# Performance work log

Hardware: AMD Instinct MI355X
Metric: run time of the kernel (lower is better)

Reference implementation:

```python
import jax, jax.numpy as jnp
import numpy as np

HEADS = 8

def setup_inputs() -> dict:
    key = jax.random.key(0)
    ks = jax.random.split(key, 7)
    B, N, M, C = 4, 2048, 2048, 512
    s = 0.02
    return {
        "hidden_states": jax.random.normal(ks[0], (B, N, C), jnp.float32),
        "encoder_states": jax.random.normal(ks[1], (B, M, C), jnp.float32),
        "Wq": jax.random.normal(ks[2], (C, C), jnp.float32) * s,
        "Wk": jax.random.normal(ks[3], (C, C), jnp.float32) * s,
        "Wv": jax.random.normal(ks[4], (C, C), jnp.float32) * s,
        "Wo": jax.random.normal(ks[5], (C, C), jnp.float32) * s,
        "bo": jnp.zeros((C,), jnp.float32),
    }

def reference(hidden_states, encoder_states, Wq, Wk, Wv, Wo, bo):
    B, N, C = hidden_states.shape
    M = encoder_states.shape[1]
    H = HEADS
    dh = C // H
    scale = dh ** -0.5  # q.shape[-1] ** -0.5 in FlashAttentionFunction / attn.scale
    # projections (to_q/to_k/to_v, no bias as in diffusers CrossAttention)
    q = (hidden_states @ Wq).reshape(B, N, H, dh).transpose(0, 2, 1, 3)   # [B,H,N,dh]
    k = (encoder_states @ Wk).reshape(B, M, H, dh).transpose(0, 2, 1, 3)  # [B,H,M,dh]
    v = (encoder_states @ Wv).reshape(B, M, H, dh).transpose(0, 2, 1, 3)  # [B,H,M,dh]
    # baddbmm(scores) -> softmax -> bmm(values); no mask, non-causal
    scores = jnp.einsum('bhnd,bhmd->bhnm', q, k) * scale                  # [B,H,N,M]
    probs = jax.nn.softmax(scores, axis=-1)
    out = jnp.einsum('bhnm,bhmd->bhnd', probs, v)                         # [B,H,N,dh]
    out = out.transpose(0, 2, 1, 3).reshape(B, N, C)                      # batch_to_head_dim
    return out @ Wo + bo                                                  # to_out[0]; to_out[1] is dropout (identity at eval)
```

## Files before the change

kernel.cpp:

```cpp
#include <hip/hip_runtime.h>
#include <stdint.h>
#include <stddef.h>

typedef __bf16 bf16x8 __attribute__((ext_vector_type(8)));
typedef float f32x4 __attribute__((ext_vector_type(4)));
typedef float f32x16 __attribute__((ext_vector_type(16)));
typedef int int4v __attribute__((ext_vector_type(4)));
typedef unsigned short u16;
typedef unsigned int u32;

__device__ __forceinline__ u16 f2bf(float f) {
    union { float f; unsigned u; } x; x.f = f;
    unsigned r = x.u + 0x7fffu + ((x.u >> 16) & 1u);
    return (u16)(r >> 16);
}

__device__ __forceinline__ float fexp2(float x) { return __builtin_amdgcn_exp2f(x); }

__device__ __forceinline__ u32 cvtpk(float lo, float hi) {
    u32 r;
    asm("v_cvt_pk_bf16_f32 %0, %1, %2" : "=v"(r) : "v"(lo), "v"(hi));
    return r;
}

__device__ __forceinline__ void perm32swap(u32& a, u32& b) {
    asm("v_permlane32_swap_b32 %0, %1" : "+v"(a), "+v"(b));
}

__device__ __forceinline__ f32x16 mfma32(bf16x8 a, bf16x8 b, f32x16 c) {
    return __builtin_amdgcn_mfma_f32_32x32x16_bf16(a, b, c, 0, 0, 0);
}

__device__ __forceinline__ void gl16(const void* g, void* l) {
    __builtin_amdgcn_global_load_lds(
        (const __attribute__((address_space(1))) void*)g,
        (__attribute__((address_space(3))) void*)l, 16, 0, 0);
}

__global__ __launch_bounds__(256) void wtrans4(
        const float* __restrict__ Wq, const float* __restrict__ Wk,
        const float* __restrict__ Wv, const float* __restrict__ Wo,
        u16* __restrict__ oq, u16* __restrict__ ok,
        u16* __restrict__ ov, u16* __restrict__ oo) {
    const int z = blockIdx.z;
    const float* W = (z == 0) ? Wq : (z == 1) ? Wk : (z == 2) ? Wv : Wo;
    u16* O = (z == 0) ? oq : (z == 1) ? ok : (z == 2) ? ov : oo;
    int t  = blockIdx.x * 256 + threadIdx.x;
    int g  = t >> 12;
    int k0 = (t >> 9) & 7;
    int n  = t & 511;
    float v[8];
#pragma unroll
    for (int j = 0; j < 8; ++j)
        v[j] = W[(size_t)(k0 * 64 + g * 8 + j) * 512 + n];
    int gs = g ^ (n & 7);
    u16* dst = O + ((size_t)(k0 * 512 + n) * 8 + gs) * 8;
    ushort4 a, b;
    a.x = f2bf(v[0]); a.y = f2bf(v[1]); a.z = f2bf(v[2]); a.w = f2bf(v[3]);
    b.x = f2bf(v[4]); b.y = f2bf(v[5]); b.z = f2bf(v[6]); b.w = f2bf(v[7]);
    *(ushort4*)dst = a;
    *(ushort4*)(dst + 4) = b;
}

__global__ __launch_bounds__(256) void gemm_qkv(
        const float* __restrict__ hidden, const float* __restrict__ enc,
        const u16* __restrict__ wq, const u16* __restrict__ wk, const u16* __restrict__ wv,
        u16* __restrict__ qo, u16* __restrict__ ko, u16* __restrict__ vo) {
    __shared__ __align__(16) u16 As[128 * 64];
    __shared__ __align__(16) u16 Bs[128 * 64];
    const int z = blockIdx.z;
    const float* A = (z == 0) ? hidden : enc;
    const u16* Bp = (z == 0) ? wq : (z == 1) ? wk : wv;
    const int tid = threadIdx.x, lane = tid & 63, wave = tid >> 6;
    const int wr = (wave >> 1) * 64, wc = (wave & 1) * 64;
    const int brow = blockIdx.x * 128, bcol = blockIdx.y * 128;
    const int lrow = lane & 15;
    const int sr = tid >> 3, sc = tid & 7;

    f32x4 acc[4][4] = {};

    for (int k0s = 0; k0s < 8; ++k0s) {
        const u16* bsrc = Bp + ((size_t)(k0s * 512 + bcol) * 64) + (size_t)(wave * 256 + lane) * 8;
#pragma unroll
        for (int i = 0; i < 4; ++i)
            gl16(bsrc + i * 512, (char*)Bs + wave * 4096 + i * 1024);
#pragma unroll
        for (int i = 0; i < 4; ++i) {
            int r = i * 32 + sr;
            const float* src = A + (size_t)(brow + r) * 512 + k0s * 64 + sc * 8;
            float4 f0 = *(const float4*)src, f1 = *(const float4*)(src + 4);
            int4v w;
            w[0] = cvtpk(f0.x, f0.y); w[1] = cvtpk(f0.z, f0.w);
            w[2] = cvtpk(f1.x, f1.y); w[3] = cvtpk(f1.z, f1.w);
            *(int4v*)((char*)As + r * 128 + ((sc ^ (r & 7)) << 4)) = w;
        }
        __syncthreads();
#pragma unroll
        for (int kc = 0; kc < 2; ++kc) {
            const int kg = kc * 4 + (lane >> 4);
            bf16x8 af[4], bfr[4];
#pragma unroll
            for (int m = 0; m < 4; ++m) {
                int r = wr + m * 16 + lrow;
                af[m] = *(const bf16x8*)((char*)As + r * 128 + ((kg ^ (r & 7)) << 4));
            }
#pragma unroll
            for (int n = 0; n < 4; ++n) {
                int r = wc + n * 16 + lrow;
                bfr[n] = *(const bf16x8*)((char*)Bs + r * 128 + ((kg ^ (r & 7)) << 4));
            }
#pragma unroll
            for (int m = 0; m < 4; ++m)
#pragma unroll
                for (int n = 0; n < 4; ++n)
                    acc[m][n] = __builtin_amdgcn_mfma_f32_16x16x32_bf16(af[m], bfr[n], acc[m][n], 0, 0, 0);
        }
        __syncthreads();
    }

#pragma unroll
    for (int m = 0; m < 4; ++m) {
        int gr0 = brow + wr + m * 16 + ((lane >> 4) << 2);
#pragma unroll
        for (int n = 0; n < 4; ++n) {
            int gc = bcol + wc + n * 16 + lrow;
            int hh = gc >> 6, d = gc & 63;
            if (z == 2) {
                int b = gr0 >> 11, mm = gr0 & 2047;
                ushort4 pk;
                pk.x = f2bf(acc[m][n][0]); pk.y = f2bf(acc[m][n][1]);
                pk.z = f2bf(acc[m][n][2]); pk.w = f2bf(acc[m][n][3]);
                *(ushort4*)(vo + ((size_t)(b * 8 + hh) * 64 + d) * 2048 + mm) = pk;
            } else {
                u16* dst = (z == 0) ? qo : ko;
                const float s = (z == 0) ? 0.125f * 1.44269504f : 1.0f;
#pragma unroll
                for (int j = 0; j < 4; ++j) {
                    int gr = gr0 + j;
                    int b = gr >> 11, nn = gr & 2047;
                    dst[((size_t)(b * 8 + hh) * 2048 + nn) * 64 + d] = f2bf(acc[m][n][j] * s);
                }
            }
        }
    }
}

__global__ __launch_bounds__(256) void gemm_out(
        const u16* __restrict__ A, const u16* __restrict__ Bp,
        const float* __restrict__ bias, float* __restrict__ out) {
    __shared__ __align__(16) u16 As[128 * 64];
    __shared__ __align__(16) u16 Bs[64 * 64];
    const int tid = threadIdx.x, lane = tid & 63, wave = tid >> 6;
    const int wr = (wave >> 1) * 64, wc = (wave & 1) * 32;
    const int brow = blockIdx.x * 128, bcol = blockIdx.y * 64;
    const int lrow = lane & 15;
    const int ar = wave * 32 + (lane >> 3), ag = lane & 7;

    f32x4 acc[4][2] = {};

    for (int k0s = 0; k0s < 8; ++k0s) {
        const u16* asrc = A + (size_t)(brow + ar) * 512 + k0s * 64 + ag * 8;
#pragma unroll
        for (int i = 0; i < 4; ++i)
            gl16(asrc + (size_t)(i * 8) * 512, (char*)As + wave * 4096 + i * 1024);
        const u16* bsrc = Bp + ((size_t)(k0s * 512 + bcol) * 64) + (size_t)(wave * 128 + lane) * 8;
#pragma unroll
        for (int i = 0; i < 2; ++i)
            gl16(bsrc + i * 512, (char*)Bs + wave * 2048 + i * 1024);
        __syncthreads();
#pragma unroll
        for (int kc = 0; kc < 2; ++kc) {
            const int kg = kc * 4 + (lane >> 4);
            bf16x8 af[4], bfr[2];
#pragma unroll
            for (int m = 0; m < 4; ++m) {
                int r = wr + m * 16 + lrow;
                af[m] = *(const bf16x8*)((char*)As + r * 128 + ((kg ^ (r & 7)) << 4));
            }
#pragma unroll
            for (int n = 0; n < 2; ++n) {
                int r = wc + n * 16 + lrow;
                bfr[n] = *(const bf16x8*)((char*)Bs + r * 128 + ((kg ^ (r & 7)) << 4));
            }
#pragma unroll
            for (int m = 0; m < 4; ++m)
#pragma unroll
                for (int n = 0; n < 2; ++n)
                    acc[m][n] = __builtin_amdgcn_mfma_f32_16x16x32_bf16(af[m], bfr[n], acc[m][n], 0, 0, 0);
        }
        __syncthreads();
    }

#pragma unroll
    for (int m = 0; m < 4; ++m) {
        int gr0 = brow + wr + m * 16 + ((lane >> 4) << 2);
#pragma unroll
        for (int n = 0; n < 2; ++n) {
            int gc = bcol + wc + n * 16 + lrow;
            float bv = bias[gc];
#pragma unroll
            for (int j = 0; j < 4; ++j)
                out[(size_t)(gr0 + j) * 512 + gc] = acc[m][n][j] + bv;
        }
    }
}

__global__ __launch_bounds__(256, 2) void flash_attn(
        const u16* __restrict__ Q, const u16* __restrict__ K,
        const u16* __restrict__ VT, u16* __restrict__ Oa) {
    __shared__ __align__(16) char smem[65536];

    const int tid  = threadIdx.x;
    const int lane = tid & 63;
    const int wave = tid >> 6;
    const int qg   = wave >> 1;
    const int half = wave & 1;
    const int ql   = lane & 31;
    const int hl   = lane >> 5;
    const int bid  = blockIdx.x;
    const int lid  = (bid & 7) * 64 + (bid >> 3);
    const int bh   = lid >> 4;
    const int qt   = lid & 15;
    const int qbase = qt * 128 + qg * 64;

    bf16x8 qf[2][4];
#pragma unroll
    for (int sq = 0; sq < 2; ++sq)
#pragma unroll
        for (int kc = 0; kc < 4; ++kc)
            qf[sq][kc] = *(const bf16x8*)(Q + ((size_t)bh * 2048 + qbase + sq * 32 + ql) * 64 + kc * 16 + hl * 8);

    const u16* Kb = K  + (size_t)bh * 131072 + ((size_t)half * 1024 + ql) * 64 + hl * 8;
    const u16* Vb = VT + (size_t)bh * 131072 + (size_t)ql * 2048 + half * 1024 + hl * 8;

#define STAGE(b_, t_) do { \
    if (qg == 0) { \
        const u16* s_ = Kb + (size_t)(t_) * 4096; \
        char* d_ = smem + (b_) * 32768 + half * 8192; \
        gl16(s_,             d_); \
        gl16(s_ + 16,        d_ + 1024); \
        gl16(s_ + 32,        d_ + 2048); \
        gl16(s_ + 48,        d_ + 3072); \
        gl16(s_ + 2048,      d_ + 4096); \
        gl16(s_ + 2048 + 16, d_ + 5120); \
        gl16(s_ + 2048 + 32, d_ + 6144); \
        gl16(s_ + 2048 + 48, d_ + 7168); \
    } else { \
        const u16* s_ = Vb + (t_) * 64; \
        char* d_ = smem + (b_) * 32768 + 16384 + half * 8192; \
        gl16(s_,              d_);           \
        gl16(s_ + 65536,      d_ + 1024);    \
        gl16(s_ + 16,         d_ + 2048);    \
        gl16(s_ + 16 + 65536, d_ + 3072);    \
        gl16(s_ + 32,         d_ + 4096);    \
        gl16(s_ + 32 + 65536, d_ + 5120);    \
        gl16(s_ + 48,         d_ + 6144);    \
        gl16(s_ + 48 + 65536, d_ + 7168);    \
    } \
} while (0)

    f32x16 acc00 = {}, acc01 = {}, acc10 = {}, acc11 = {};
    float ls[2][4] = {};

    STAGE(0, 0);
    __syncthreads();

    for (int t = 0; t < 16; ++t) {
        const int b = t & 1;
        if (t < 15) STAGE(b ^ 1, t + 1);

#pragma unroll
        for (int ks = 0; ks < 2; ++ks) {
            const u16* Kt = (const u16*)(smem + b * 32768 + half * 8192 + ks * 4096);
            const u16* Vt = (const u16*)(smem + b * 32768 + 16384 + half * 8192 + ks * 4096);
            bf16x8 kf[4], vf[2][2];
#pragma unroll
            for (int kc = 0; kc < 4; ++kc)
                kf[kc] = *(const bf16x8*)(Kt + kc * 512 + lane * 8);
#pragma unroll
            for (int jl = 0; jl < 2; ++jl)
#pragma unroll
                for (int dh2 = 0; dh2 < 2; ++dh2)
                    vf[jl][dh2] = *(const bf16x8*)(Vt + (jl * 2 + dh2) * 512 + lane * 8);

            f32x16 st0 = {}, st1 = {};
            __builtin_amdgcn_s_setprio(1);
#pragma unroll
            for (int kc = 0; kc < 4; ++kc) {
                st0 = mfma32(kf[kc], qf[0][kc], st0);
                st1 = mfma32(kf[kc], qf[1][kc], st1);
            }
            __builtin_amdgcn_s_setprio(0);

#pragma unroll
            for (int r = 0; r < 16; r += 4) {
                st0[r]   = fexp2(st0[r]);   ls[0][0] += st0[r];
                st0[r+1] = fexp2(st0[r+1]); ls[0][1] += st0[r+1];
                st0[r+2] = fexp2(st0[r+2]); ls[0][2] += st0[r+2];
                st0[r+3] = fexp2(st0[r+3]); ls[0][3] += st0[r+3];
                st1[r]   = fexp2(st1[r]);   ls[1][0] += st1[r];
                st1[r+1] = fexp2(st1[r+1]); ls[1][1] += st1[r+1];
                st1[r+2] = fexp2(st1[r+2]); ls[1][2] += st1[r+2];
                st1[r+3] = fexp2(st1[r+3]); ls[1][3] += st1[r+3];
            }

            __builtin_amdgcn_s_setprio(1);
#pragma unroll
            for (int jl = 0; jl < 2; ++jl) {
                u32 A0 = cvtpk(st0[8*jl+0], st0[8*jl+1]);
                u32 A1 = cvtpk(st0[8*jl+2], st0[8*jl+3]);
                u32 B0 = cvtpk(st0[8*jl+4], st0[8*jl+5]);
                u32 B1 = cvtpk(st0[8*jl+6], st0[8*jl+7]);
                perm32swap(A0, B0);
                perm32swap(A1, B1);
                union { bf16x8 v; u32 u[4]; } bb0;
                bb0.u[0] = A0; bb0.u[1] = A1; bb0.u[2] = B0; bb0.u[3] = B1;
                acc00 = mfma32(vf[jl][0], bb0.v, acc00);
                acc01 = mfma32(vf[jl][1], bb0.v, acc01);
                u32 C0 = cvtpk(st1[8*jl+0], st1[8*jl+1]);
                u32 C1 = cvtpk(st1[8*jl+2], st1[8*jl+3]);
                u32 D0 = cvtpk(st1[8*jl+4], st1[8*jl+5]);
                u32 D1 = cvtpk(st1[8*jl+6], st1[8*jl+7]);
                perm32swap(C0, D0);
                perm32swap(C1, D1);
                union { bf16x8 v; u32 u[4]; } bb1;
                bb1.u[0] = C0; bb1.u[1] = C1; bb1.u[2] = D0; bb1.u[3] = D1;
                acc10 = mfma32(vf[jl][0], bb1.v, acc10);
                acc11 = mfma32(vf[jl][1], bb1.v, acc11);
            }
            __builtin_amdgcn_s_setprio(0);
        }
        __syncthreads();
    }
#undef STAGE

    float lsum0 = (ls[0][0] + ls[0][1]) + (ls[0][2] + ls[0][3]);
    float lsum1 = (ls[1][0] + ls[1][1]) + (ls[1][2] + ls[1][3]);
    lsum0 += __shfl_xor(lsum0, 32);
    lsum1 += __shfl_xor(lsum1, 32);

    float* CB = (float*)smem;
    float* LS = (float*)(smem + 32768);

#define PUBQ(sq, A0, A1, LSV) do { \
    int qq = (sq) * 32 + ql; \
    float* R = CB + qg * 4096 + qq * 64; \
    _Pragma("unroll") \
    for (int rg = 0; rg < 4; ++rg) { \
        int g0 = (2 * rg + hl) ^ (qq & 15); \
        *(f32x4*)(R + g0 * 4) = f32x4{A0[4*rg], A0[4*rg+1], A0[4*rg+2], A0[4*rg+3]}; \
        int g1 = (8 + 2 * rg + hl) ^ (qq & 15); \
        *(f32x4*)(R + g1 * 4) = f32x4{A1[4*rg], A1[4*rg+1], A1[4*rg+2], A1[4*rg+3]}; \
    } \
    if (hl == 0) LS[qg * 64 + qq] = LSV; \
} while (0)

#define REDQ(sq, A0, A1, LSV) do { \
    int qq = (sq) * 32 + ql; \
    const float* R = CB + qg * 4096 + qq * 64; \
    _Pragma("unroll") \
    for (int rg = 0; rg < 4; ++rg) { \
        int g0 = (2 * rg + hl) ^ (qq & 15); \
        f32x4 v0 = *(const f32x4*)(R + g0 * 4); \
        A0[4*rg] += v0[0]; A0[4*rg+1] += v0[1]; A0[4*rg+2] += v0[2]; A0[4*rg+3] += v0[3]; \
        int g1 = (8 + 2 * rg + hl) ^ (qq & 15); \
        f32x4 v1 = *(const f32x4*)(R + g1 * 4); \
        A1[4*rg] += v1[0]; A1[4*rg+1] += v1[1]; A1[4*rg+2] += v1[2]; A1[4*rg+3] += v1[3]; \
    } \
    LSV += LS[qg * 64 + qq]; \
} while (0)

    if (half == 1) {
        PUBQ(0, acc00, acc01, lsum0);
        PUBQ(1, acc10, acc11, lsum1);
    }
    __syncthreads();
    if (half == 0) {
        REDQ(0, acc00, acc01, lsum0);
        REDQ(1, acc10, acc11, lsum1);
        float inv0 = 1.0f / lsum0, inv1 = 1.0f / lsum1;
        int b_ = bh >> 3, hd = bh & 7;
#define STOQ(sq, A0, A1, INV) do { \
        int qrow = qbase + (sq) * 32 + ql; \
        u16* orow = Oa + ((size_t)b_ * 2048 + qrow) * 512 + hd * 64; \
        _Pragma("unroll") \
        for (int rg = 0; rg < 4; ++rg) { \
            int d00 = ((rg ^ (qrow & 7)) << 3) + hl * 4; \
            ushort4 p0; \
            p0.x = f2bf(A0[4*rg] * INV);   p0.y = f2bf(A0[4*rg+1] * INV); \
            p0.z = f2bf(A0[4*rg+2] * INV); p0.w = f2bf(A0[4*rg+3] * INV); \
            *(ushort4*)(orow + d00) = p0; \
            int d01 = (((4 + rg) ^ (qrow & 7)) << 3) + hl * 4; \
            ushort4 p1; \
            p1.x = f2bf(A1[4*rg] * INV);   p1.y = f2bf(A1[4*rg+1] * INV); \
            p1.z = f2bf(A1[4*rg+2] * INV); p1.w = f2bf(A1[4*rg+3] * INV); \
            *(ushort4*)(orow + d01) = p1; \
        } \
} while (0)
        STOQ(0, acc00, acc01, inv0);
        STOQ(1, acc10, acc11, inv1);
#undef STOQ
    }
#undef PUBQ
#undef REDQ
}

extern "C" void kernel_launch(void* const* d_in, const int* in_sizes, int n_in,
                              void* d_out, int out_size, void* d_ws, size_t ws_size,
                              hipStream_t stream) {
    const float* hidden = (const float*)d_in[0];
    const float* enc    = (const float*)d_in[1];
    const float* Wq     = (const float*)d_in[2];
    const float* Wk     = (const float*)d_in[3];
    const float* Wv     = (const float*)d_in[4];
    const float* Wo     = (const float*)d_in[5];
    const float* bo     = (const float*)d_in[6];
    float* out = (float*)d_out;

    char* ws = (char*)d_ws;
    const size_t MB = 1ull << 20;
    u16* q_bf  = (u16*)(ws + 0 * MB);
    u16* k_bf  = (u16*)(ws + 8 * MB);
    u16* vt_bf = (u16*)(ws + 16 * MB);
    u16* at_bf = (u16*)(ws + 24 * MB);
    u16* wq_t  = (u16*)(ws + 32 * MB);
    u16* wk_t  = (u16*)(ws + 32 * MB + 512 * 1024);
    u16* wv_t  = (u16*)(ws + 33 * MB);
    u16* wo_t  = (u16*)(ws + 33 * MB + 512 * 1024);

    dim3 wg(128, 1, 4);
    wtrans4<<<wg, 256, 0, stream>>>(Wq, Wk, Wv, Wo, wq_t, wk_t, wv_t, wo_t);

    dim3 qkvg(64, 4, 3);
    gemm_qkv<<<qkvg, 256, 0, stream>>>(hidden, enc, wq_t, wk_t, wv_t, q_bf, k_bf, vt_bf);

    flash_attn<<<512, 256, 0, stream>>>(q_bf, k_bf, vt_bf, at_bf);

    dim3 og(64, 8);
    gemm_out<<<og, 256, 0, stream>>>(at_bf, wo_t, bo, out);
}
```

Measured before the change: 91.08 us.

## Pre-pack K and V into MFMA fragment layout and shrink attention LDS footprint

The QKV projection now writes K and V directly in the per-lane fragment order the attention kernel consumes, so each staging step is four contiguous 1KB copies per wave instead of strided gathers. The attention kernel halves its per-iteration tile (32 iterations of one sub-step), cutting shared memory from 64KB to about 33KB and raising launch bounds to allow four blocks per CU. This aims to improve global load coalescing and occupancy, at the cost of twice as many barriers and scattered 2-byte stores in the K write-out.

After: 220.3 us. +141.9%, slower.

```diff
diff --git a/kernel.cpp b/kernel.cpp
--- a/kernel.cpp
+++ b/kernel.cpp
@@ -125,21 +125,33 @@
         for (int n = 0; n < 4; ++n) {
             int gc = bcol + wc + n * 16 + lrow;
             int hh = gc >> 6, d = gc & 63;
-            if (z == 2) {
-                int b = gr0 >> 11, mm = gr0 & 2047;
+            int b = gr0 >> 11;
+            int bh2 = b * 8 + hh;
+            if (z == 0) {
+                int nn = gr0 & 2047;
+#pragma unroll
+                for (int j = 0; j < 4; ++j)
+                    qo[((size_t)bh2 * 2048 + nn + j) * 64 + d] =
+                        f2bf(acc[m][n][j] * (0.125f * 1.44269504f));
+            } else if (z == 1) {
+                int kc2 = d >> 4, hl2 = (d >> 3) & 1, e = d & 7;
+#pragma unroll
+                for (int j = 0; j < 4; ++j) {
+                    int nn = (gr0 & 2047) + j;
+                    size_t off = (((size_t)bh2 * 64 + (nn >> 5)) * 4 + kc2) * 512
+                               + (size_t)((nn & 31) + 32 * hl2) * 8 + e;
+                    ko[off] = f2bf(acc[m][n][j]);
+                }
+            } else {
+                int nn0 = gr0 & 2047;
+                int slice = ((nn0 >> 4) & 1) * 2 + (d >> 5);
+                int lanev = (d & 31) + 32 * ((nn0 >> 3) & 1);
+                size_t off = (((size_t)bh2 * 64 + (nn0 >> 5)) * 4 + slice) * 512
+                           + (size_t)lanev * 8 + (nn0 & 7);
                 ushort4 pk;
                 pk.x = f2bf(acc[m][n][0]); pk.y = f2bf(acc[m][n][1]);
                 pk.z = f2bf(acc[m][n][2]); pk.w = f2bf(acc[m][n][3]);
-                *(ushort4*)(vo + ((size_t)(b * 8 + hh) * 64 + d) * 2048 + mm) = pk;
-            } else {
-                u16* dst = (z == 0) ? qo : ko;
-                const float s = (z == 0) ? 0.125f * 1.44269504f : 1.0f;
-#pragma unroll
-                for (int j = 0; j < 4; ++j) {
-                    int gr = gr0 + j;
-                    int b = gr >> 11, nn = gr & 2047;
-                    dst[((size_t)(b * 8 + hh) * 2048 + nn) * 64 + d] = f2bf(acc[m][n][j] * s);
-                }
+                *(ushort4*)(vo + off) = pk;
             }
         }
     }
@@ -205,10 +217,10 @@
     }
 }
 
-__global__ __launch_bounds__(256, 2) void flash_attn(
-        const u16* __restrict__ Q, const u16* __restrict__ K,
-        const u16* __restrict__ VT, u16* __restrict__ Oa) {
-    __shared__ __align__(16) char smem[65536];
+__global__ __launch_bounds__(256, 4) void flash_attn(
+        const u16* __restrict__ KQ, const u16* __restrict__ KP,
+        const u16* __restrict__ VP, u16* __restrict__ Oa) {
+    __shared__ __align__(16) char smem[33280];
 
     const int tid  = threadIdx.x;
     const int lane = tid & 63;
@@ -228,35 +240,18 @@
     for (int sq = 0; sq < 2; ++sq)
 #pragma unroll
         for (int kc = 0; kc < 4; ++kc)
-            qf[sq][kc] = *(const bf16x8*)(Q + ((size_t)bh * 2048 + qbase + sq * 32 + ql) * 64 + kc * 16 + hl * 8);
-
-    const u16* Kb = K  + (size_t)bh * 131072 + ((size_t)half * 1024 + ql) * 64 + hl * 8;
-    const u16* Vb = VT + (size_t)bh * 131072 + (size_t)ql * 2048 + half * 1024 + hl * 8;
+            qf[sq][kc] = *(const bf16x8*)(KQ + ((size_t)bh * 2048 + qbase + sq * 32 + ql) * 64 + kc * 16 + hl * 8);
+
+    const u16* Pb = (qg == 0 ? KP : VP) + ((size_t)bh * 64 + half * 32) * 2048 + lane * 8;
+    char* dst0 = smem + half * 8192 + (qg == 0 ? 0 : 4096);
 
 #define STAGE(b_, t_) do { \
-    if (qg == 0) { \
-        const u16* s_ = Kb + (size_t)(t_) * 4096; \
-        char* d_ = smem + (b_) * 32768 + half * 8192; \
-        gl16(s_,             d_); \
-        gl16(s_ + 16,        d_ + 1024); \
-        gl16(s_ + 32,        d_ + 2048); \
-        gl16(s_ + 48,        d_ + 3072); \
-        gl16(s_ + 2048,      d_ + 4096); \
-        gl16(s_ + 2048 + 16, d_ + 5120); \
-        gl16(s_ + 2048 + 32, d_ + 6144); \
-        gl16(s_ + 2048 + 48, d_ + 7168); \
-    } else { \
-        const u16* s_ = Vb + (t_) * 64; \
-        char* d_ = smem + (b_) * 32768 + 16384 + half * 8192; \
-        gl16(s_,              d_);           \
-        gl16(s_ + 65536,      d_ + 1024);    \
-        gl16(s_ + 16,         d_ + 2048);    \
-        gl16(s_ + 16 + 65536, d_ + 3072);    \
-        gl16(s_ + 32,         d_ + 4096);    \
-        gl16(s_ + 32 + 65536, d_ + 5120);    \
-        gl16(s_ + 48,         d_ + 6144);    \
-        gl16(s_ + 48 + 65536, d_ + 7168);    \
-    } \
+    const u16* s_ = Pb + (size_t)(t_) * 2048; \
+    char* d_ = dst0 + (b_) * 16384; \
+    gl16(s_,        d_); \
+    gl16(s_ + 512,  d_ + 1024); \
+    gl16(s_ + 1024, d_ + 2048); \
+    gl16(s_ + 1536, d_ + 3072); \
 } while (0)
 
     f32x16 acc00 = {}, acc01 = {}, acc10 = {}, acc11 = {};
@@ -265,71 +260,69 @@
     STAGE(0, 0);
     __syncthreads();
 
-    for (int t = 0; t < 16; ++t) {
+    for (int t = 0; t < 32; ++t) {
         const int b = t & 1;
-        if (t < 15) STAGE(b ^ 1, t + 1);
-
-#pragma unroll
-        for (int ks = 0; ks < 2; ++ks) {
-            const u16* Kt = (const u16*)(smem + b * 32768 + half * 8192 + ks * 4096);
-            const u16* Vt = (const u16*)(smem + b * 32768 + 16384 + half * 8192 + ks * 4096);
-            bf16x8 kf[4], vf[2][2];
-#pragma unroll
-            for (int kc = 0; kc < 4; ++kc)
-                kf[kc] = *(const bf16x8*)(Kt + kc * 512 + lane * 8);
-#pragma unroll
-            for (int jl = 0; jl < 2; ++jl)
-#pragma unroll
-                for (int dh2 = 0; dh2 < 2; ++dh2)
-                    vf[jl][dh2] = *(const bf16x8*)(Vt + (jl * 2 + dh2) * 512 + lane * 8);
-
-            f32x16 st0 = {}, st1 = {};
-            __builtin_amdgcn_s_setprio(1);
-#pragma unroll
-            for (int kc = 0; kc < 4; ++kc) {
-                st0 = mfma32(kf[kc], qf[0][kc], st0);
-                st1 = mfma32(kf[kc], qf[1][kc], st1);
-            }
-            __builtin_amdgcn_s_setprio(0);
-
-#pragma unroll
-            for (int r = 0; r < 16; r += 4) {
-                st0[r]   = fexp2(st0[r]);   ls[0][0] += st0[r];
-                st0[r+1] = fexp2(st0[r+1]); ls[0][1] += st0[r+1];
-                st0[r+2] = fexp2(st0[r+2]); ls[0][2] += st0[r+2];
-                st0[r+3] = fexp2(st0[r+3]); ls[0][3] += st0[r+3];
-                st1[r]   = fexp2(st1[r]);   ls[1][0] += st1[r];
-                st1[r+1] = fexp2(st1[r+1]); ls[1][1] += st1[r+1];
-                st1[r+2] = fexp2(st1[r+2]); ls[1][2] += st1[r+2];
-                st1[r+3] = fexp2(st1[r+3]); ls[1][3] += st1[r+3];
-            }
-
-            __builtin_amdgcn_s_setprio(1);
-#pragma unroll
-            for (int jl = 0; jl < 2; ++jl) {
-                u32 A0 = cvtpk(st0[8*jl+0], st0[8*jl+1]);
-                u32 A1 = cvtpk(st0[8*jl+2], st0[8*jl+3]);
-                u32 B0 = cvtpk(st0[8*jl+4], st0[8*jl+5]);
-                u32 B1 = cvtpk(st0[8*jl+6], st0[8*jl+7]);
-                perm32swap(A0, B0);
-                perm32swap(A1, B1);
-                union { bf16x8 v; u32 u[4]; } bb0;
-                bb0.u[0] = A0; bb0.u[1] = A1; bb0.u[2] = B0; bb0.u[3] = B1;
-                acc00 = mfma32(vf[jl][0], bb0.v, acc00);
-                acc01 = mfma32(vf[jl][1], bb0.v, acc01);
-                u32 C0 = cvtpk(st1[8*jl+0], st1[8*jl+1]);
-                u32 C1 = cvtpk(st1[8*jl+2], st1[8*jl+3]);
-                u32 D0 = cvtpk(st1[8*jl+4], st1[8*jl+5]);
-                u32 D1 = cvtpk(st1[8*jl+6], st1[8*jl+7]);
-                perm32swap(C0, D0);
-                perm32swap(C1, D1);
-                union { bf16x8 v; u32 u[4]; } bb1;
-                bb1.u[0] = C0; bb1.u[1] = C1; bb1.u[2] = D0; bb1.u[3] = D1;
-                acc10 = mfma32(vf[jl][0], bb1.v, acc10);
-                acc11 = mfma32(vf[jl][1], bb1.v, acc11);
-            }
-            __builtin_amdgcn_s_setprio(0);
-        }
+        if (t < 31) STAGE(b ^ 1, t + 1);
+
+        const u16* Kt = (const u16*)(smem + b * 16384 + half * 8192);
+        const u16* Vt = Kt + 2048;
+        bf16x8 kf[4], vf[2][2];
+#pragma unroll
+        for (int kc = 0; kc < 4; ++kc)
+            kf[kc] = *(const bf16x8*)(Kt + kc * 512 + lane * 8);
+#pragma unroll
+        for (int jl = 0; jl < 2; ++jl)
+#pragma unroll
+            for (int dh2 = 0; dh2 < 2; ++dh2)
+                vf[jl][dh2] = *(const bf16x8*)(Vt + (jl * 2 + dh2) * 512 + lane * 8);
+
+        f32x16 st0 = {}, st1 = {};
+        __builtin_amdgcn_s_setprio(1);
+#pragma unroll
+        for (int kc = 0; kc < 4; ++kc) {
+            st0 = mfma32(kf[kc], qf[0][kc], st0);
+            st1 = mfma32(kf[kc], qf[1][kc], st1);
+        }
+        __builtin_amdgcn_s_setprio(0);
+
+#pragma unroll
+        for (int r = 0; r < 16; r += 4) {
+            st0[r]   = fexp2(st0[r]);   ls[0][0] += st0[r];
+            st0[r+1] = fexp2(st0[r+1]); ls[0][1] += st0[r+1];
+            st0[r+2] = fexp2(st0[r+2]); ls[0][2] += st0[r+2];
+            st0[r+3] = fexp2(st0[r+3]); ls[0][3] += st0[r+3];
+            st1[r]   = fexp2(st1[r]);   ls[1][0] += st1[r];
+            st1[r+1] = fexp2(st1[r+1]); ls[1][1] += st1[r+1];
+            st1[r+2] = fexp2(st1[r+2]); ls[1][2] += st1[r+2];
+            st1[r+3] = fexp2(st1[r+3]); ls[1][3] += st1[r+3];
+        }
+
+        __builtin_amdgcn_s_setprio(1);
+#pragma unroll
+        for (int jl = 0; jl < 2; ++jl) {
+            u32 A0 = cvtpk(st0[8*jl+0], st0[8*jl+1]);
+            u32 A1 = cvtpk(st0[8*jl+2], st0[8*jl+3]);
+            u32 B0 = cvtpk(st0[8*jl+4], st0[8*jl+5]);
+            u32 B1 = cvtpk(st0[8*jl+6], st0[8*jl+7]);
+            perm32swap(A0, B0);
+            perm32swap(A1, B1);
+            union { bf16x8 v; u32 u[4]; } bb0;
+            bb0.u[0] = A0; bb0.u[1] = A1; bb0.u[2] = B0; bb0.u[3] = B1;
+            acc00 = mfma32(vf[jl][0], bb0.v, acc00);
+            acc01 = mfma32(vf[jl][1], bb0.v, acc01);
+            u32 C0 = cvtpk(st1[8*jl+0], st1[8*jl+1]);
+            u32 C1 = cvtpk(st1[8*jl+2], st1[8*jl+3]);
+            u32 D0 = cvtpk(st1[8*jl+4], st1[8*jl+5]);
+            u32 D1 = cvtpk(st1[8*jl+6], st1[8*jl+7]);
+            perm32swap(C0, D0);
+            perm32swap(C1, D1);
+            union { bf16x8 v; u32 u[4]; } bb1;
+            bb1.u[0] = C0; bb1.u[1] = C1; bb1.u[2] = D0; bb1.u[3] = D1;
+            acc10 = mfma32(vf[jl][0], bb1.v, acc10);
+            acc11 = mfma32(vf[jl][1], bb1.v, acc11);
+        }
+        __builtin_amdgcn_s_setprio(0);
+
         __syncthreads();
     }
 #undef STAGE
@@ -420,8 +413,8 @@
     char* ws = (char*)d_ws;
     const size_t MB = 1ull << 20;
     u16* q_bf  = (u16*)(ws + 0 * MB);
-    u16* k_bf  = (u16*)(ws + 8 * MB);
-    u16* vt_bf = (u16*)(ws + 16 * MB);
+    u16* kp_bf = (u16*)(ws + 8 * MB);
+    u16* vp_bf = (u16*)(ws + 16 * MB);
     u16* at_bf = (u16*)(ws + 24 * MB);
     u16* wq_t  = (u16*)(ws + 32 * MB);
     u16* wk_t  = (u16*)(ws + 32 * MB + 512 * 1024);
@@ -432,9 +425,9 @@
     wtrans4<<<wg, 256, 0, stream>>>(Wq, Wk, Wv, Wo, wq_t, wk_t, wv_t, wo_t);
 
     dim3 qkvg(64, 4, 3);
-    gemm_qkv<<<qkvg, 256, 0, stream>>>(hidden, enc, wq_t, wk_t, wv_t, q_bf, k_bf, vt_bf);
-
-    flash_attn<<<512, 256, 0, stream>>>(q_bf, k_bf, vt_bf, at_bf);
+    gemm_qkv<<<qkvg, 256, 0, stream>>>(hidden, enc, wq_t, wk_t, wv_t, q_bf, kp_bf, vp_bf);
+
+    flash_attn<<<512, 256, 0, stream>>>(q_bf, kp_bf, vp_bf, at_bf);
 
     dim3 og(64, 8);
     gemm_out<<<og, 256, 0, stream>>>(at_bf, wo_t, bo, out);
```
